# Optimization experiments

Measured on AMD Instinct MI355X. Metric: run time of the kernel, lower is better.

## Reference

```python
import jax, jax.numpy as jnp
import numpy as np

NUM_LAYERS = 16
ALPHA = 1.0
EPS = 1e-20

def setup_inputs() -> dict:
    key = jax.random.key(0)
    k1, k2, k3, k4 = jax.random.split(key, 4)
    B, S, M, G = 8, 9, 8, 512
    M2 = M * M
    return {
        "dict_real": jax.random.normal(k1, (B, S, M2, G), dtype=jnp.float32),
        "dict_imag": jax.random.normal(k2, (B, S, M2, G), dtype=jnp.float32),
        "cov_real": jax.random.normal(k3, (B, S, M, M), dtype=jnp.float32),
        "cov_imag": jax.random.normal(k4, (B, S, M, M), dtype=jnp.float32),
    }

def reference(dict_real, dict_imag, cov_real, cov_imag):
    D = (dict_real + 1j * dict_imag).astype(jnp.complex64)   # (B,S,M2,G) dictionary_band
    C = (cov_real + 1j * cov_imag).astype(jnp.complex64)     # (B,S,M,M) covariance matrix
    B, S, M, _ = C.shape
    G = D.shape[-1]
    # covariance_vector = cov.transpose(2,3).reshape(B,S,M2,1)
    r = jnp.swapaxes(C, 2, 3).reshape(B, S, M * M, 1)
    Dh = jnp.conj(jnp.swapaxes(D, 2, 3))                     # (B,S,G,M2)
    DhD = jnp.matmul(Dh, D)                                  # (B,S,G,G) Hermitian PSD
    Dhr = jnp.matmul(Dh, r)                                  # (B,S,G,1)
    # initial spectrum: real part, L2-normalized over grid dim
    res = jnp.real(Dhr).astype(jnp.float32)
    res = res / (jnp.linalg.norm(res, axis=2, keepdims=True) + EPS)
    # gamma = 1 / max|eig(D^H D)|; Hermitian PSD so eigvalsh gives same max magnitude
    eig = jnp.linalg.eigvalsh(DhD)                           # (B,S,G) real
    gamma = 1.0 / jnp.max(jnp.abs(eig), axis=2, keepdims=True)        # (B,S,1)
    lam = 0.5 * jnp.max(jnp.abs(Dhr), axis=2, keepdims=True).reshape(B, S, 1)
    theta = (ALPHA * lam * gamma).reshape(B, S, 1, 1)
    g = gamma.reshape(B, S, 1, 1).astype(jnp.complex64)
    I = jnp.eye(G, dtype=jnp.complex64)
    Wt = I - g * DhD                                         # (B,S,G,G)
    Wer = g * Dhr                                            # We @ r, constant per layer

    def step(res_c, _):
        s = jnp.matmul(Wt, res_c.astype(jnp.complex64)) + Wer
        res_new = jax.nn.relu(jnp.abs(s) - theta)            # soft-shrinkage on magnitude
        return res_new, res_new

    res_final, res_all = jax.lax.scan(step, res, None, length=NUM_LAYERS)
    result_init_all = jnp.moveaxis(res_all, 0, 2)            # (B,S,L,G,1)

    def minmax_norm(x):
        lo = jnp.min(x, axis=2, keepdims=True)
        hi = jnp.max(x, axis=2, keepdims=True)
        return (x - lo) / (hi - lo + EPS)

    result_ave = minmax_norm(jnp.mean(res_final, axis=1, keepdims=True).astype(jnp.float32))
    result = minmax_norm(res_final)
    return (result, result_ave, result_init_all)
```

## Files before the change

### kernel.cpp

```cpp
#include <hip/hip_runtime.h>
#include <math.h>

#define N_SQ   7
#define INV_P  (1.0f / 256.0f)
#define EPS_F  1e-20f
#define PH     72
#define PQ     67

typedef _Float16 h2    __attribute__((ext_vector_type(2)));
typedef _Float16 f16x8 __attribute__((ext_vector_type(8)));
typedef float    f32x4 __attribute__((ext_vector_type(4)));

__device__ inline float cdot2(h2 a, h2 b, float c) {
#if __has_builtin(__builtin_amdgcn_fdot2)
    return __builtin_amdgcn_fdot2(a, b, c, false);
#else
    return c + (float)a.x * (float)b.x + (float)a.y * (float)b.y;
#endif
}
__device__ inline h2 bch2(unsigned int x) { return __builtin_bit_cast(h2, x); }
__device__ inline h2 bch2f(float x)       { return __builtin_bit_cast(h2, x); }
__device__ inline float bcf(h2 x)         { return __builtin_bit_cast(float, x); }


__global__ __launch_bounds__(512, 1) void ista_main_kernel(
    const float* __restrict__ Dre, const float* __restrict__ Dim,
    const float* __restrict__ Cre, const float* __restrict__ Cim,
    float* __restrict__ out, float* __restrict__ ws)
{
    const int bs = blockIdx.x;
    const int t  = threadIdx.x;
    const int wv = t >> 6;
    const int ln = t & 63;
    const int c16 = ln & 15;
    const int qd  = ln >> 4;
    const float* __restrict__ dre = Dre + (size_t)bs * 32768;
    const float* __restrict__ dim = Dim + (size_t)bs * 32768;

    __shared__ __align__(16) float uBuf[9216];
    _Float16* ShRe = (_Float16*)uBuf;
    _Float16* ShIm = (_Float16*)uBuf + 64 * PH;
    float*    Q1   = uBuf + 4608;
    float*    sUp  = uBuf;
    float*    sHu  = uBuf + 1024;
    _Float16* sResH = (_Float16*)(uBuf + 1152);
    __shared__ __align__(16) float s_r[128];
    __shared__ float s_red[16];
    __shared__ float s_scal[8];

    if (t < 64) {
        int i = t >> 3, j = t & 7;
        s_r[2 * t]     = Cre[bs * 64 + j * 8 + i];
        s_r[2 * t + 1] = Cim[bs * 64 + j * 8 + i];
    }
    __syncthreads();

    float dhr_re = 0.f, dhr_im = 0.f;
    h2 dV[64];
    #pragma unroll
    for (int m = 0; m < 64; ++m) {
        float ar = dre[m * 512 + t], ai = dim[m * 512 + t];
        dV[m] = h2{(_Float16)ar, (_Float16)ai};
        float rr = s_r[2 * m], ri = s_r[2 * m + 1];
        dhr_re += ar * rr + ai * ri;
        dhr_im += ar * ri - ai * rr;
    }
    {
        float sv = dhr_re * dhr_re;
        float mv = sqrtf(dhr_re * dhr_re + dhr_im * dhr_im);
        for (int off = 32; off; off >>= 1) {
            sv += __shfl_down(sv, off, 64);
            mv = fmaxf(mv, __shfl_down(mv, off, 64));
        }
        if (ln == 0) { s_red[wv] = sv; s_red[8 + wv] = mv; }
        __syncthreads();
        if (t == 0) {
            float ss = 0.f, mm = 0.f;
            for (int k = 0; k < 8; ++k) { ss += s_red[k]; mm = fmaxf(mm, s_red[8 + k]); }
            s_scal[7] = ss; s_scal[2] = mm;
        }
        __syncthreads();
    }
    float res_g = dhr_re / (sqrtf(s_scal[7]) + EPS_F);

    const int tau0 = 2 * wv, tau1 = 2 * wv + 1;
    const int I0 = tau0 >> 2, J0 = tau0 & 3;
    const int I1 = tau1 >> 2, J1 = tau1 & 3;

    auto epilogue = [&](f32x4 P0, f32x4 Qa0, f32x4 P1, f32x4 Qa1, bool first, bool last) {
        #pragma unroll
        for (int r = 0; r < 4; ++r) {
            Q1[(I0 * 16 + qd * 4 + r) * PQ + J0 * 16 + c16] = Qa0[r];
            Q1[(I1 * 16 + qd * 4 + r) * PQ + J1 * 16 + c16] = Qa1[r];
        }
        float dv = 0.f;
        if (I0 == J0) {
            #pragma unroll
            for (int r = 0; r < 4; ++r) if (qd * 4 + r == c16) dv = fmaxf(dv, fabsf(P0[r]));
        }
        if (I1 == J1) {
            #pragma unroll
            for (int r = 0; r < 4; ++r) if (qd * 4 + r == c16) dv = fmaxf(dv, fabsf(P1[r]));
        }
        for (int off = 32; off; off >>= 1) dv = fmaxf(dv, __shfl_down(dv, off, 64));
        if (ln == 0) s_red[wv] = dv;
        __syncthreads();
        if (t == 0) {
            float m = 0.f;
            for (int k = 0; k < 8; ++k) m = fmaxf(m, s_red[k]);
            s_scal[3] = first ? logf(m) : 2.f * s_scal[3] + logf(m);
            s_scal[4] = 1.f / m;
        }
        __syncthreads();
        float ic = s_scal[4];
        float ci0[4], ci1[4];
        #pragma unroll
        for (int r = 0; r < 4; ++r) {
            ci0[r] = Qa0[r] - Q1[(J0 * 16 + c16) * PQ + I0 * 16 + qd * 4 + r];
            ci1[r] = Qa1[r] - Q1[(J1 * 16 + c16) * PQ + I1 * 16 + qd * 4 + r];
        }
        if (!last) {
            #pragma unroll
            for (int r = 0; r < 4; ++r) {
                ShRe[(I0 * 16 + qd * 4 + r) * PH + J0 * 16 + c16] = (_Float16)(P0[r] * ic);
                ShIm[(I0 * 16 + qd * 4 + r) * PH + J0 * 16 + c16] = (_Float16)(ci0[r] * ic);
                ShRe[(I1 * 16 + qd * 4 + r) * PH + J1 * 16 + c16] = (_Float16)(P1[r] * ic);
                ShIm[(I1 * 16 + qd * 4 + r) * PH + J1 * 16 + c16] = (_Float16)(ci1[r] * ic);
            }
            __syncthreads();
        } else {
            float fr = 0.f;
            #pragma unroll
            for (int r = 0; r < 4; ++r)
                fr += P0[r] * P0[r] + ci0[r] * ci0[r] + P1[r] * P1[r] + ci1[r] * ci1[r];
            fr *= ic * ic;
            for (int off = 32; off; off >>= 1) fr += __shfl_down(fr, off, 64);
            if (ln == 0) s_red[wv] = fr;
            __syncthreads();
            if (t == 0) {
                float fsum = 0.f;
                for (int k = 0; k < 8; ++k) fsum += s_red[k];
                float loglam = (2.f * s_scal[3] + logf(fsum)) * INV_P;
                float gamma = expf(-loglam);
                s_scal[0] = gamma;
                s_scal[1] = 0.5f * s_scal[2] * gamma;
            }
            __syncthreads();
        }
    };

    h2 du_re[32], du_im[32];
    f32x4 gP0 = {0.f, 0.f, 0.f, 0.f}, gQ0 = {0.f, 0.f, 0.f, 0.f};
    f32x4 gP1 = {0.f, 0.f, 0.f, 0.f}, gQ1 = {0.f, 0.f, 0.f, 0.f};
    {
        const int srow = t >> 4;
        const int scb  = (t & 15) * 4;
        float4 pr0, pi0, pr1, pi1;
        pr0 = *(const float4*)&dre[srow * 512 + scb];
        pi0 = *(const float4*)&dim[srow * 512 + scb];
        pr1 = *(const float4*)&dre[(srow + 32) * 512 + scb];
        pi1 = *(const float4*)&dim[(srow + 32) * 512 + scb];
        for (int ch = 0; ch < 8; ++ch) {
            *(h2*)&ShRe[srow * PH + scb]     = h2{(_Float16)pr0.x, (_Float16)pr0.y};
            *(h2*)&ShRe[srow * PH + scb + 2] = h2{(_Float16)pr0.z, (_Float16)pr0.w};
            *(h2*)&ShIm[srow * PH + scb]     = h2{(_Float16)pi0.x, (_Float16)pi0.y};
            *(h2*)&ShIm[srow * PH + scb + 2] = h2{(_Float16)pi0.z, (_Float16)pi0.w};
            *(h2*)&ShRe[(srow + 32) * PH + scb]     = h2{(_Float16)pr1.x, (_Float16)pr1.y};
            *(h2*)&ShRe[(srow + 32) * PH + scb + 2] = h2{(_Float16)pr1.z, (_Float16)pr1.w};
            *(h2*)&ShIm[(srow + 32) * PH + scb]     = h2{(_Float16)pi1.x, (_Float16)pi1.y};
            *(h2*)&ShIm[(srow + 32) * PH + scb + 2] = h2{(_Float16)pi1.z, (_Float16)pi1.w};
            if (ch < 7) {
                int gc = (ch + 1) * 64;
                pr0 = *(const float4*)&dre[srow * 512 + gc + scb];
                pi0 = *(const float4*)&dim[srow * 512 + gc + scb];
                pr1 = *(const float4*)&dre[(srow + 32) * 512 + gc + scb];
                pi1 = *(const float4*)&dim[(srow + 32) * 512 + gc + scb];
            }
            __syncthreads();
            #pragma unroll
            for (int ks = 0; ks < 64; ks += 32) {
                f16x8 arI0 = *(const f16x8*)&ShRe[(I0 * 16 + c16) * PH + ks + qd * 8];
                f16x8 aiI0 = *(const f16x8*)&ShIm[(I0 * 16 + c16) * PH + ks + qd * 8];
                f16x8 arJ0 = *(const f16x8*)&ShRe[(J0 * 16 + c16) * PH + ks + qd * 8];
                f16x8 aiJ0 = *(const f16x8*)&ShIm[(J0 * 16 + c16) * PH + ks + qd * 8];
                gP0 = __builtin_amdgcn_mfma_f32_16x16x32_f16(arI0, arJ0, gP0, 0, 0, 0);
                gP0 = __builtin_amdgcn_mfma_f32_16x16x32_f16(aiI0, aiJ0, gP0, 0, 0, 0);
                gQ0 = __builtin_amdgcn_mfma_f32_16x16x32_f16(aiI0, arJ0, gQ0, 0, 0, 0);
                f16x8 arI1 = *(const f16x8*)&ShRe[(I1 * 16 + c16) * PH + ks + qd * 8];
                f16x8 aiI1 = *(const f16x8*)&ShIm[(I1 * 16 + c16) * PH + ks + qd * 8];
                f16x8 arJ1 = *(const f16x8*)&ShRe[(J1 * 16 + c16) * PH + ks + qd * 8];
                f16x8 aiJ1 = *(const f16x8*)&ShIm[(J1 * 16 + c16) * PH + ks + qd * 8];
                gP1 = __builtin_amdgcn_mfma_f32_16x16x32_f16(arI1, arJ1, gP1, 0, 0, 0);
                gP1 = __builtin_amdgcn_mfma_f32_16x16x32_f16(aiI1, aiJ1, gP1, 0, 0, 0);
                gQ1 = __builtin_amdgcn_mfma_f32_16x16x32_f16(aiI1, arJ1, gQ1, 0, 0, 0);
            }
            if (ch == wv) {
                #pragma unroll
                for (int c = 0; c < 8; ++c) {
                    uint4 aw = *(const uint4*)&ShRe[ln * PH + 8 * c];
                    du_re[4 * c + 0] = bch2(aw.x); du_re[4 * c + 1] = bch2(aw.y);
                    du_re[4 * c + 2] = bch2(aw.z); du_re[4 * c + 3] = bch2(aw.w);
                    uint4 bw = *(const uint4*)&ShIm[ln * PH + 8 * c];
                    du_im[4 * c + 0] = bch2(bw.x); du_im[4 * c + 1] = bch2(bw.y);
                    du_im[4 * c + 2] = bch2(bw.z); du_im[4 * c + 3] = bch2(bw.w);
                }
            }
            __syncthreads();
        }
    }
    epilogue(gP0, gQ0, gP1, gQ1, true, false);

    for (int sq = 0; sq < N_SQ; ++sq) {
        f32x4 P0 = {0.f, 0.f, 0.f, 0.f}, Qa0 = {0.f, 0.f, 0.f, 0.f};
        f32x4 P1 = {0.f, 0.f, 0.f, 0.f}, Qa1 = {0.f, 0.f, 0.f, 0.f};
        #pragma unroll
        for (int ks = 0; ks < 64; ks += 32) {
            f16x8 arI0 = *(const f16x8*)&ShRe[(I0 * 16 + c16) * PH + ks + qd * 8];
            f16x8 aiI0 = *(const f16x8*)&ShIm[(I0 * 16 + c16) * PH + ks + qd * 8];
            f16x8 arJ0 = *(const f16x8*)&ShRe[(J0 * 16 + c16) * PH + ks + qd * 8];
            f16x8 aiJ0 = *(const f16x8*)&ShIm[(J0 * 16 + c16) * PH + ks + qd * 8];
            P0  = __builtin_amdgcn_mfma_f32_16x16x32_f16(arI0, arJ0, P0, 0, 0, 0);
            P0  = __builtin_amdgcn_mfma_f32_16x16x32_f16(aiI0, aiJ0, P0, 0, 0, 0);
            Qa0 = __builtin_amdgcn_mfma_f32_16x16x32_f16(aiI0, arJ0, Qa0, 0, 0, 0);
            f16x8 arI1 = *(const f16x8*)&ShRe[(I1 * 16 + c16) * PH + ks + qd * 8];
            f16x8 aiI1 = *(const f16x8*)&ShIm[(I1 * 16 + c16) * PH + ks + qd * 8];
            f16x8 arJ1 = *(const f16x8*)&ShRe[(J1 * 16 + c16) * PH + ks + qd * 8];
            f16x8 aiJ1 = *(const f16x8*)&ShIm[(J1 * 16 + c16) * PH + ks + qd * 8];
            P1  = __builtin_amdgcn_mfma_f32_16x16x32_f16(arI1, arJ1, P1, 0, 0, 0);
            P1  = __builtin_amdgcn_mfma_f32_16x16x32_f16(aiI1, aiJ1, P1, 0, 0, 0);
            Qa1 = __builtin_amdgcn_mfma_f32_16x16x32_f16(aiI1, arJ1, Qa1, 0, 0, 0);
        }
        epilogue(P0, Qa0, P1, Qa1, false, sq == N_SQ - 1);
    }

    const float gamma = s_scal[0];
    const float theta = s_scal[1];
    float* out_init = out + 40960 + (size_t)bs * 8192;
    const int resh_base = 64 * wv;

    for (int l = 0; l < 16; ++l) {
        sResH[t] = (_Float16)res_g;
        float upR = 0.f, upI = 0.f;
        #pragma unroll
        for (int c = 0; c < 8; ++c) {
            uint4 rw = *(const uint4*)&sResH[resh_base + 8 * c];
            h2 r0 = bch2(rw.x), r1 = bch2(rw.y), r2 = bch2(rw.z), r3 = bch2(rw.w);
            upR = cdot2(du_re[4 * c + 0], r0, upR);  upI = cdot2(du_im[4 * c + 0], r0, upI);
            upR = cdot2(du_re[4 * c + 1], r1, upR);  upI = cdot2(du_im[4 * c + 1], r1, upI);
            upR = cdot2(du_re[4 * c + 2], r2, upR);  upI = cdot2(du_im[4 * c + 2], r2, upI);
            upR = cdot2(du_re[4 * c + 3], r3, upR);  upI = cdot2(du_im[4 * c + 3], r3, upI);
        }
        *(float2*)&sUp[(wv * 64 + ln) * 2] = make_float2(upR, upI);
        __syncthreads();
        if (wv == 0) {
            float ufR = 0.f, ufI = 0.f;
            #pragma unroll
            for (int w8 = 0; w8 < 8; ++w8) {
                float2 p = *(const float2*)&sUp[(w8 * 64 + ln) * 2];
                ufR += p.x; ufI += p.y;
            }
            h2 hu1 = h2{(_Float16)ufR, (_Float16)ufI};
            h2 hu2 = h2{(_Float16)ufI, (_Float16)(-ufR)};
            *(float2*)&sHu[2 * ln] = make_float2(bcf(hu1), bcf(hu2));
        }
        __syncthreads();
        float wR = 0.f, wI = 0.f;
        #pragma unroll
        for (int mm = 0; mm < 32; ++mm) {
            float4 hq = *(const float4*)&sHu[4 * mm];
            wR = cdot2(dV[2 * mm],     bch2f(hq.x), wR);
            wI = cdot2(dV[2 * mm],     bch2f(hq.y), wI);
            wR = cdot2(dV[2 * mm + 1], bch2f(hq.z), wR);
            wI = cdot2(dV[2 * mm + 1], bch2f(hq.w), wI);
        }
        float sre = res_g + gamma * (dhr_re - wR);
        float sim = gamma * (dhr_im - wI);
        float mag = sqrtf(sre * sre + sim * sim);
        res_g = fmaxf(mag - theta, 0.f);
        out_init[l * 512 + t] = res_g;
    }

    {
        float mn = res_g, mx = res_g;
        for (int off = 32; off; off >>= 1) {
            mn = fminf(mn, __shfl_down(mn, off, 64));
            mx = fmaxf(mx, __shfl_down(mx, off, 64));
        }
        if (ln == 0) { s_red[wv] = mn; s_red[8 + wv] = mx; }
        __syncthreads();
        if (t == 0) {
            float a = s_red[0], b2 = s_red[8];
            for (int k = 1; k < 8; ++k) { a = fminf(a, s_red[k]); b2 = fmaxf(b2, s_red[8 + k]); }
            s_scal[5] = a; s_scal[6] = b2;
        }
        __syncthreads();
        out[bs * 512 + t] = (res_g - s_scal[5]) / (s_scal[6] - s_scal[5] + EPS_F);
        ws[bs * 512 + t] = res_g;
    }
}

__global__ __launch_bounds__(512) void ista_ave_kernel(
    const float* __restrict__ ws, float* __restrict__ out)
{
    const int b = blockIdx.x;
    const int g = threadIdx.x;
    __shared__ float s_red[16];
    __shared__ float s_scal[2];
    float acc = 0.f;
    #pragma unroll
    for (int s = 0; s < 9; ++s) acc += ws[(b * 9 + s) * 512 + g];
    acc *= (1.f / 9.f);
    float mn = acc, mx = acc;
    for (int off = 32; off; off >>= 1) {
        mn = fminf(mn, __shfl_down(mn, off, 64));
        mx = fmaxf(mx, __shfl_down(mx, off, 64));
    }
    if ((g & 63) == 0) { s_red[g >> 6] = mn; s_red[8 + (g >> 6)] = mx; }
    __syncthreads();
    if (g == 0) {
        float a = s_red[0], b2 = s_red[8];
        for (int k = 1; k < 8; ++k) { a = fminf(a, s_red[k]); b2 = fmaxf(b2, s_red[8 + k]); }
        s_scal[0] = a; s_scal[1] = b2;
    }
    __syncthreads();
    out[36864 + b * 512 + g] = (acc - s_scal[0]) / (s_scal[1] - s_scal[0] + EPS_F);
}

extern "C" void kernel_launch(void* const* d_in, const int* in_sizes, int n_in,
                              void* d_out, int out_size, void* d_ws, size_t ws_size,
                              hipStream_t stream) {
    const float* Dre = (const float*)d_in[0];
    const float* Dim = (const float*)d_in[1];
    const float* Cre = (const float*)d_in[2];
    const float* Cim = (const float*)d_in[3];
    float* out = (float*)d_out;
    float* ws  = (float*)d_ws;

    ista_main_kernel<<<72, 512, 0, stream>>>(Dre, Dim, Cre, Cim, out, ws);
    ista_ave_kernel<<<8, 512, 0, stream>>>(ws, out);
}
```

Before: 112.6 us.

## Fuse batch-average kernel via atomic last-block counter and defer Dhr computation

Replaces the second kernel launch with a last-block-done pattern: each block increments a per-batch atomic counter, and the ninth block to finish computes the mean over S and its min-max normalisation. A hipMemsetAsync resets the counters before the launch. The D^H r computation and its register-resident dV load are also moved after the Gram/eigenvalue phase, which shortens register live ranges during the MFMA section, and theta is now computed once gamma and the Dhr maximum are both known. The change removes one kernel launch but adds a memset, atomics and threadfences.

```diff
diff --git a/kernel.cpp b/kernel.cpp
--- a/kernel.cpp
+++ b/kernel.cpp
@@ -26,7 +26,7 @@
 __global__ __launch_bounds__(512, 1) void ista_main_kernel(
     const float* __restrict__ Dre, const float* __restrict__ Dim,
     const float* __restrict__ Cre, const float* __restrict__ Cim,
-    float* __restrict__ out, float* __restrict__ ws)
+    float* __restrict__ out, float* __restrict__ ws, int* __restrict__ cnt)
 {
     const int bs = blockIdx.x;
     const int t  = threadIdx.x;
@@ -47,6 +47,7 @@
     __shared__ __align__(16) float s_r[128];
     __shared__ float s_red[16];
     __shared__ float s_scal[8];
+    __shared__ int s_flag;
 
     if (t < 64) {
         int i = t >> 3, j = t & 7;
@@ -54,34 +55,6 @@
         s_r[2 * t + 1] = Cim[bs * 64 + j * 8 + i];
     }
     __syncthreads();
-
-    float dhr_re = 0.f, dhr_im = 0.f;
-    h2 dV[64];
-    #pragma unroll
-    for (int m = 0; m < 64; ++m) {
-        float ar = dre[m * 512 + t], ai = dim[m * 512 + t];
-        dV[m] = h2{(_Float16)ar, (_Float16)ai};
-        float rr = s_r[2 * m], ri = s_r[2 * m + 1];
-        dhr_re += ar * rr + ai * ri;
-        dhr_im += ar * ri - ai * rr;
-    }
-    {
-        float sv = dhr_re * dhr_re;
-        float mv = sqrtf(dhr_re * dhr_re + dhr_im * dhr_im);
-        for (int off = 32; off; off >>= 1) {
-            sv += __shfl_down(sv, off, 64);
-            mv = fmaxf(mv, __shfl_down(mv, off, 64));
-        }
-        if (ln == 0) { s_red[wv] = sv; s_red[8 + wv] = mv; }
-        __syncthreads();
-        if (t == 0) {
-            float ss = 0.f, mm = 0.f;
-            for (int k = 0; k < 8; ++k) { ss += s_red[k]; mm = fmaxf(mm, s_red[8 + k]); }
-            s_scal[7] = ss; s_scal[2] = mm;
-        }
-        __syncthreads();
-    }
-    float res_g = dhr_re / (sqrtf(s_scal[7]) + EPS_F);
 
     const int tau0 = 2 * wv, tau1 = 2 * wv + 1;
     const int I0 = tau0 >> 2, J0 = tau0 & 3;
@@ -141,9 +114,7 @@
                 float fsum = 0.f;
                 for (int k = 0; k < 8; ++k) fsum += s_red[k];
                 float loglam = (2.f * s_scal[3] + logf(fsum)) * INV_P;
-                float gamma = expf(-loglam);
-                s_scal[0] = gamma;
-                s_scal[1] = 0.5f * s_scal[2] * gamma;
+                s_scal[0] = expf(-loglam);
             }
             __syncthreads();
         }
@@ -233,6 +204,35 @@
         epilogue(P0, Qa0, P1, Qa1, false, sq == N_SQ - 1);
     }
 
+    float dhr_re = 0.f, dhr_im = 0.f;
+    h2 dV[64];
+    #pragma unroll
+    for (int m = 0; m < 64; ++m) {
+        float ar = dre[m * 512 + t], ai = dim[m * 512 + t];
+        dV[m] = h2{(_Float16)ar, (_Float16)ai};
+        float rr = s_r[2 * m], ri = s_r[2 * m + 1];
+        dhr_re += ar * rr + ai * ri;
+        dhr_im += ar * ri - ai * rr;
+    }
+    {
+        float sv = dhr_re * dhr_re;
+        float mv = sqrtf(dhr_re * dhr_re + dhr_im * dhr_im);
+        for (int off = 32; off; off >>= 1) {
+            sv += __shfl_down(sv, off, 64);
+            mv = fmaxf(mv, __shfl_down(mv, off, 64));
+        }
+        if (ln == 0) { s_red[wv] = sv; s_red[8 + wv] = mv; }
+        __syncthreads();
+        if (t == 0) {
+            float ss = 0.f, mmx = 0.f;
+            for (int k = 0; k < 8; ++k) { ss += s_red[k]; mmx = fmaxf(mmx, s_red[8 + k]); }
+            s_scal[7] = ss; s_scal[2] = mmx;
+            s_scal[1] = 0.5f * mmx * s_scal[0];
+        }
+        __syncthreads();
+    }
+    float res_g = dhr_re / (sqrtf(s_scal[7]) + EPS_F);
+
     const float gamma = s_scal[0];
     const float theta = s_scal[1];
     float* out_init = out + 40960 + (size_t)bs * 8192;
@@ -296,6 +296,30 @@
         __syncthreads();
         out[bs * 512 + t] = (res_g - s_scal[5]) / (s_scal[6] - s_scal[5] + EPS_F);
         ws[bs * 512 + t] = res_g;
+    }
+
+    if (cnt != nullptr) {
+        const int b = bs / 9;
+        __threadfence();
+        if (t == 0) s_flag = (atomicAdd(&cnt[b], 1) == 8);
+        __syncthreads();
+        if (!s_flag) return;
+        __threadfence();
+        float acc = 0.f;
+        #pragma unroll
+        for (int s = 0; s < 9; ++s) acc += ws[(b * 9 + s) * 512 + t];
+        acc *= (1.f / 9.f);
+        float mn = acc, mx = acc;
+        for (int off = 32; off; off >>= 1) {
+            mn = fminf(mn, __shfl_down(mn, off, 64));
+            mx = fmaxf(mx, __shfl_down(mx, off, 64));
+        }
+        if (ln == 0) { s_red[wv] = mn; s_red[8 + wv] = mx; }
+        __syncthreads();
+        float lo = s_red[0], hi = s_red[8];
+        #pragma unroll
+        for (int k = 1; k < 8; ++k) { lo = fminf(lo, s_red[k]); hi = fmaxf(hi, s_red[8 + k]); }
+        out[36864 + b * 512 + t] = (acc - lo) / (hi - lo + EPS_F);
     }
 }
 
@@ -336,6 +360,11 @@
     float* out = (float*)d_out;
     float* ws  = (float*)d_ws;
 
-    ista_main_kernel<<<72, 512, 0, stream>>>(Dre, Dim, Cre, Cim, out, ws);
-    ista_ave_kernel<<<8, 512, 0, stream>>>(ws, out);
+    const size_t cnt_off = (size_t)36864 * 4;
+    const bool fuse = ws_size >= cnt_off + 8 * sizeof(int);
+    int* cnt = fuse ? (int*)((char*)d_ws + cnt_off) : nullptr;
+    if (fuse) hipMemsetAsync(cnt, 0, 8 * sizeof(int), stream);
+
+    ista_main_kernel<<<72, 512, 0, stream>>>(Dre, Dim, Cre, Cim, out, ws, cnt);
+    if (!fuse) ista_ave_kernel<<<8, 512, 0, stream>>>(ws, out);
 }
```

After: 124.3 us. +10.4%, slower.
